# Optimization experiments

Measured on AMD Instinct MI355X. Metric: run time of the kernel, lower is better.

## Reference

```python
import jax, jax.numpy as jnp
import numpy as np

N, E = 50000, 600000
DIN, H, DOUT = 128, 128, 64


def setup_inputs() -> dict:
    key = jax.random.key(0)
    ks = jax.random.split(key, 8)
    x = jax.random.normal(ks[0], (N, DIN), dtype=jnp.float32)
    edge_index = jax.random.randint(ks[1], (2, E), 0, N, dtype=jnp.int64)
    s1 = 1.0 / np.sqrt(DIN)
    s2 = 1.0 / np.sqrt(H)
    # PyG SAGEConv: lin_l (on aggregated neighbors, with bias), lin_r (on root, no bias)
    w1_l = jax.random.uniform(ks[2], (DIN, H), jnp.float32, -s1, s1)
    b1 = jnp.zeros((H,), jnp.float32)
    w1_r = jax.random.uniform(ks[3], (DIN, H), jnp.float32, -s1, s1)
    w2_l = jax.random.uniform(ks[4], (H, DOUT), jnp.float32, -s2, s2)
    b2 = jnp.zeros((DOUT,), jnp.float32)
    w2_r = jax.random.uniform(ks[5], (H, DOUT), jnp.float32, -s2, s2)
    return {"x": x, "edge_index": edge_index, "w1_l": w1_l, "b1": b1,
            "w1_r": w1_r, "w2_l": w2_l, "b2": b2, "w2_r": w2_r}


def _sage_conv(h, src, dst, w_l, b, w_r):
    # mean-aggregate neighbor features: gather by src, scatter-sum to dst
    agg = jax.ops.segment_sum(h[src], dst, num_segments=N)  # [N, d]
    deg = jax.ops.segment_sum(jnp.ones((src.shape[0],), h.dtype), dst,
                              num_segments=N)
    mean = agg / jnp.maximum(deg, 1.0)[:, None]
    return mean @ w_l + b + h @ w_r


def reference(x, edge_index, w1_l, b1, w1_r, w2_l, b2, w2_r):
    src, dst = edge_index[0], edge_index[1]
    h = jax.nn.relu(_sage_conv(x, src, dst, w1_l, b1, w1_r))
    return _sage_conv(h, src, dst, w2_l, b2, w2_r)
```

## Files before the change

kernel.cpp:

```cpp
#include <hip/hip_runtime.h>

#define N_NODES 50000
#define N_EDGES 600000
#define DIN 128
#define HD 128
#define DOUT 64
#define NBINS 196
#define BUFCAP 32
#define MAXBIN 6144

typedef float f32x4 __attribute__((ext_vector_type(4)));
typedef short bf16x8 __attribute__((ext_vector_type(8)));

__device__ __forceinline__ unsigned short f2bf(float f) {
    unsigned u = __float_as_uint(f);
    unsigned r = (u + 0x7FFFu + ((u >> 16) & 1u)) >> 16;
    return (unsigned short)r;
}

__global__ __launch_bounds__(256) void cursorinit_kernel(int* __restrict__ binCursor) {
    if (threadIdx.x < NBINS) binCursor[threadIdx.x] = threadIdx.x * MAXBIN;
}

__global__ __launch_bounds__(256) void mega_kernel(const int* __restrict__ ei,
                                                   int* __restrict__ binCursor,
                                                   unsigned* __restrict__ gbuf,
                                                   const float* __restrict__ x,
                                                   unsigned short* __restrict__ xb,
                                                   const float* __restrict__ w1l,
                                                   const float* __restrict__ w1r,
                                                   const float* __restrict__ w2l,
                                                   const float* __restrict__ w2r,
                                                   unsigned short* __restrict__ bfr) {
    int gid = blockIdx.x;
    if (gid < 256) {
        __shared__ unsigned buf[NBINS][BUFCAP];
        __shared__ int cnt[NBINS];
        for (int i = threadIdx.x; i < NBINS; i += 256) cnt[i] = 0;
        __syncthreads();
        const int per = (N_EDGES + 255) / 256;
        int beg = gid * per;
        int end = min(beg + per, N_EDGES);
        for (int base = beg; base < end; base += 256) {
            int e = base + threadIdx.x;
            if (e < end) {
                int s = ei[e];
                int d = ei[N_EDGES + e];
                int bin = d >> 8;
                unsigned entry = ((unsigned)(d & 255) << 17) | (unsigned)s;
                int pos = atomicAdd(&cnt[bin], 1);
                if (pos < BUFCAP) buf[bin][pos] = entry;
                else { int g = atomicAdd(&binCursor[bin], 1); gbuf[g] = entry; }
            }
            __syncthreads();
            if (threadIdx.x < NBINS) {
                int b = threadIdx.x;
                int n = cnt[b]; if (n > BUFCAP) n = BUFCAP;
                int k = n & ~15;
                if (k > 0) {
                    int g = atomicAdd(&binCursor[b], k);
                    for (int j = 0; j < k; j++) gbuf[g + j] = buf[b][j];
                    for (int j = 0; j < n - k; j++) buf[b][j] = buf[b][k + j];
                    cnt[b] = n - k;
                } else {
                    cnt[b] = n;
                }
            }
            __syncthreads();
        }
        if (threadIdx.x < NBINS) {
            int b = threadIdx.x;
            int n = cnt[b]; if (n > BUFCAP) n = BUFCAP;
            if (n > 0) {
                int g = atomicAdd(&binCursor[b], n);
                for (int j = 0; j < n; j++) gbuf[g + j] = buf[b][j];
            }
        }
    } else if (gid < 6506) {
        int i = (gid - 256) * 256 + threadIdx.x;
        float4 v = ((const float4*)x)[i];
        ushort4 o;
        o.x = f2bf(v.x); o.y = f2bf(v.y); o.z = f2bf(v.z); o.w = f2bf(v.w);
        ((ushort4*)xb)[i] = o;
    } else {
        int tid = (gid - 6506) * 256 + threadIdx.x;
        int a = tid >> 14;
        int r = tid & 16383;
        int j = r & 7, lane = (r >> 3) & 63, kc = (r >> 9) & 3, ct = r >> 11;
        int k = kc * 32 + ((lane >> 4) << 3) + j;
        int c = (ct << 4) + (lane & 15);
        float v;
        if (a == 0) v = w1l[k * HD + c];
        else if (a == 1) v = w1r[k * HD + c];
        else v = (c < 64) ? w2l[k * DOUT + c] : w2r[k * DOUT + (c - 64)];
        bfr[tid] = f2bf(v);
    }
}

__global__ __launch_bounds__(256) void binsort_kernel(unsigned* __restrict__ gbuf,
                                                      const int* __restrict__ binCursor,
                                                      int* __restrict__ row_ptr,
                                                      int* __restrict__ row_end) {
    __shared__ unsigned ebuf[MAXBIN];
    __shared__ int hist[256];
    __shared__ int cur[256];
    __shared__ int ws[4];
    const int bin = blockIdx.x;
    const int base = bin * MAXBIN;
    int n = binCursor[bin] - base;
    if (n > MAXBIN) n = MAXBIN;
    unsigned* src = gbuf + base;
    for (int i = threadIdx.x; i < n; i += 256) ebuf[i] = src[i];
    hist[threadIdx.x] = 0;
    __syncthreads();
    for (int i = threadIdx.x; i < n; i += 256) atomicAdd(&hist[ebuf[i] >> 17], 1);
    __syncthreads();
    const int lane = threadIdx.x & 63, wid = threadIdx.x >> 6;
    int v = hist[threadIdx.x];
    int incl = v;
#pragma unroll
    for (int off = 1; off < 64; off <<= 1) {
        int t = __shfl_up(incl, (unsigned)off, 64);
        if (lane >= off) incl += t;
    }
    if (lane == 63) ws[wid] = incl;
    __syncthreads();
    int woff = 0;
    for (int w = 0; w < wid; w++) woff += ws[w];
    int excl = woff + incl - v;
    cur[threadIdx.x] = excl;
    int node = bin * 256 + threadIdx.x;
    if (node < N_NODES) {
        row_ptr[node] = base + excl;
        row_end[node] = base + excl + v;
    }
    __syncthreads();
    for (int i = threadIdx.x; i < n; i += 256) {
        unsigned e = ebuf[i];
        int pos = atomicAdd(&cur[e >> 17], 1);
        src[pos] = e & 0x1FFFFu;
    }
}

__global__ __launch_bounds__(256) void gather1_kernel(const int* __restrict__ row_ptr,
                                                      const int* __restrict__ row_end,
                                                      const int* __restrict__ csr,
                                                      const unsigned short* __restrict__ xb,
                                                      unsigned short* __restrict__ meanb) {
    int node = blockIdx.x * 4 + (threadIdx.x >> 6);
    if (node >= N_NODES) return;
    const int lane = threadIdx.x & 63;
    const int g = lane >> 4;
    const int sl = lane & 15;
    int beg = row_ptr[node], end = row_end[node];
    float acc[8] = {0.f, 0.f, 0.f, 0.f, 0.f, 0.f, 0.f, 0.f};
    for (int base = beg + g; base < end; base += 12) {
        int i1 = base + 4, i2 = base + 8;
        int s0 = csr[base];
        int s1 = csr[i1 < end ? i1 : base];
        int s2 = csr[i2 < end ? i2 : base];
        uint4 u0 = *(const uint4*)(xb + (size_t)s0 * DIN + sl * 8);
        uint4 u1 = *(const uint4*)(xb + (size_t)s1 * DIN + sl * 8);
        uint4 u2 = *(const uint4*)(xb + (size_t)s2 * DIN + sl * 8);
        if (i1 >= end) u1 = (uint4){0u, 0u, 0u, 0u};
        if (i2 >= end) u2 = (uint4){0u, 0u, 0u, 0u};
        acc[0] += __uint_as_float(u0.x << 16) + __uint_as_float(u1.x << 16) + __uint_as_float(u2.x << 16);
        acc[1] += __uint_as_float(u0.x & 0xffff0000u) + __uint_as_float(u1.x & 0xffff0000u) + __uint_as_float(u2.x & 0xffff0000u);
        acc[2] += __uint_as_float(u0.y << 16) + __uint_as_float(u1.y << 16) + __uint_as_float(u2.y << 16);
        acc[3] += __uint_as_float(u0.y & 0xffff0000u) + __uint_as_float(u1.y & 0xffff0000u) + __uint_as_float(u2.y & 0xffff0000u);
        acc[4] += __uint_as_float(u0.z << 16) + __uint_as_float(u1.z << 16) + __uint_as_float(u2.z << 16);
        acc[5] += __uint_as_float(u0.z & 0xffff0000u) + __uint_as_float(u1.z & 0xffff0000u) + __uint_as_float(u2.z & 0xffff0000u);
        acc[6] += __uint_as_float(u0.w << 16) + __uint_as_float(u1.w << 16) + __uint_as_float(u2.w << 16);
        acc[7] += __uint_as_float(u0.w & 0xffff0000u) + __uint_as_float(u1.w & 0xffff0000u) + __uint_as_float(u2.w & 0xffff0000u);
    }
#pragma unroll
    for (int i = 0; i < 8; i++) {
        acc[i] += __shfl_xor(acc[i], 16, 64);
        acc[i] += __shfl_xor(acc[i], 32, 64);
    }
    float r0, r1;
    if (g == 0)      { r0 = acc[0]; r1 = acc[1]; }
    else if (g == 1) { r0 = acc[2]; r1 = acc[3]; }
    else if (g == 2) { r0 = acc[4]; r1 = acc[5]; }
    else             { r0 = acc[6]; r1 = acc[7]; }
    float invd = 1.0f / fmaxf((float)(end - beg), 1.0f);
    ushort2 r; r.x = f2bf(r0 * invd); r.y = f2bf(r1 * invd);
    *(ushort2*)(meanb + (size_t)node * DIN + sl * 8 + g * 2) = r;
}

__global__ __launch_bounds__(256) void fused_kernel(
    const unsigned short* __restrict__ meanb, const unsigned short* __restrict__ xb,
    const unsigned short* __restrict__ B1a, const unsigned short* __restrict__ B1b,
    const unsigned short* __restrict__ B2,
    const float* __restrict__ b1, const float* __restrict__ b2,
    unsigned short* __restrict__ pb, float* __restrict__ out) {
    __shared__ unsigned short Am[64 * 128];
    __shared__ unsigned short Ax[64 * 128];
    const int block0 = blockIdx.x * 64;
    const int tid = threadIdx.x;
    const int lane = tid & 63;
    const int wtile = tid >> 6;

    uint4 mv[4], xv[4];
#pragma unroll
    for (int i = 0; i < 4; i++) {
        int f = tid + i * 256;
        int row = f >> 4;
        int c8 = f & 15;
        int rg = block0 + row;
        if (rg >= N_NODES) rg = N_NODES - 1;
        mv[i] = *(const uint4*)(meanb + (size_t)rg * DIN + c8 * 8);
        xv[i] = *(const uint4*)(xb + (size_t)rg * DIN + c8 * 8);
    }

    f32x4 acc[8];
#pragma unroll
    for (int t = 0; t < 8; t++) acc[t] = (f32x4){0.f, 0.f, 0.f, 0.f};

#pragma unroll
    for (int i = 0; i < 4; i++) {
        int f = tid + i * 256;
        int row = f >> 4;
        int c8 = f & 15;
        int byte = row * 256 + ((c8 * 16) ^ ((row & 7) << 4));
        *(uint4*)((char*)Am + byte) = mv[i];
        *(uint4*)((char*)Ax + byte) = xv[i];
    }

    auto compute = [&](const unsigned short* __restrict__ As,
                       const unsigned short* __restrict__ Bf) {
        const int arow = wtile * 16 + (lane & 15);
        const int swz = (arow & 7) << 4;
#pragma unroll
        for (int kc = 0; kc < 4; kc++) {
            int byte = arow * 256 + ((kc * 64 + ((lane >> 4) << 4)) ^ swz);
            bf16x8 a = *(const bf16x8*)((const char*)As + byte);
#pragma unroll
            for (int ct = 0; ct < 8; ct++) {
                bf16x8 b = *(const bf16x8*)(Bf + ((((ct << 2) + kc) << 6) + lane) * 8);
                acc[ct] = __builtin_amdgcn_mfma_f32_16x16x32_bf16(a, b, acc[ct], 0, 0, 0);
            }
        }
    };

    __syncthreads();
    compute(Am, B1a);
    compute(Ax, B1b);

    {
        const int r0 = wtile * 16 + ((lane >> 4) << 2);
#pragma unroll
        for (int ct = 0; ct < 8; ct++) {
            int col = (ct << 4) + (lane & 15);
            float bv = b1[col];
#pragma unroll
            for (int r = 0; r < 4; r++) {
                float v = fmaxf(acc[ct][r] + bv, 0.f);
                int row = r0 + r;
                int byte = row * 256 + ((col * 2) ^ ((row & 7) << 4));
                *(unsigned short*)((char*)Am + byte) = f2bf(v);
            }
            acc[ct] = (f32x4){0.f, 0.f, 0.f, 0.f};
        }
    }
    compute(Am, B2);

    {
        const int r0 = wtile * 16 + ((lane >> 4) << 2);
#pragma unroll
        for (int ct = 0; ct < 8; ct++) {
            int col = (ct << 4) + (lane & 15);
#pragma unroll
            for (int r = 0; r < 4; r++) {
                int node = block0 + r0 + r;
                if (node < N_NODES) {
                    if (ct < 4) pb[(size_t)node * DOUT + col] = f2bf(acc[ct][r]);
                    else out[(size_t)node * DOUT + (col - 64)] = acc[ct][r] + b2[col - 64];
                }
            }
        }
    }
}

__global__ __launch_bounds__(256) void gather2_kernel(const int* __restrict__ row_ptr,
                                                      const int* __restrict__ row_end,
                                                      const int* __restrict__ csr,
                                                      const unsigned short* __restrict__ pb,
                                                      float* __restrict__ out) {
    int node = blockIdx.x * 4 + (threadIdx.x >> 6);
    if (node >= N_NODES) return;
    const int lane = threadIdx.x & 63;
    const int g = lane >> 3;
    const int sl = lane & 7;
    int beg = row_ptr[node], end = row_end[node];
    float acc[8] = {0.f, 0.f, 0.f, 0.f, 0.f, 0.f, 0.f, 0.f};
    for (int base = beg + g; base < end; base += 16) {
        int i1 = base + 8;
        int s0 = csr[base];
        int s1 = csr[i1 < end ? i1 : base];
        uint4 u0 = *(const uint4*)(pb + (size_t)s0 * DOUT + sl * 8);
        uint4 u1 = *(const uint4*)(pb + (size_t)s1 * DOUT + sl * 8);
        if (i1 >= end) u1 = (uint4){0u, 0u, 0u, 0u};
        acc[0] += __uint_as_float(u0.x << 16) + __uint_as_float(u1.x << 16);
        acc[1] += __uint_as_float(u0.x & 0xffff0000u) + __uint_as_float(u1.x & 0xffff0000u);
        acc[2] += __uint_as_float(u0.y << 16) + __uint_as_float(u1.y << 16);
        acc[3] += __uint_as_float(u0.y & 0xffff0000u) + __uint_as_float(u1.y & 0xffff0000u);
        acc[4] += __uint_as_float(u0.z << 16) + __uint_as_float(u1.z << 16);
        acc[5] += __uint_as_float(u0.z & 0xffff0000u) + __uint_as_float(u1.z & 0xffff0000u);
        acc[6] += __uint_as_float(u0.w << 16) + __uint_as_float(u1.w << 16);
        acc[7] += __uint_as_float(u0.w & 0xffff0000u) + __uint_as_float(u1.w & 0xffff0000u);
    }
#pragma unroll
    for (int i = 0; i < 8; i++) {
        acc[i] += __shfl_xor(acc[i], 8, 64);
        acc[i] += __shfl_xor(acc[i], 16, 64);
        acc[i] += __shfl_xor(acc[i], 32, 64);
    }
    float r;
    if (g == 0)      r = acc[0];
    else if (g == 1) r = acc[1];
    else if (g == 2) r = acc[2];
    else if (g == 3) r = acc[3];
    else if (g == 4) r = acc[4];
    else if (g == 5) r = acc[5];
    else if (g == 6) r = acc[6];
    else             r = acc[7];
    float invd = 1.0f / fmaxf((float)(end - beg), 1.0f);
    int d = sl * 8 + g;
    out[(size_t)node * DOUT + d] += r * invd;
}

extern "C" void kernel_launch(void* const* d_in, const int* in_sizes, int n_in,
                              void* d_out, int out_size, void* d_ws, size_t ws_size,
                              hipStream_t stream) {
    const float* x   = (const float*)d_in[0];
    const int*   ei  = (const int*)d_in[1];
    const float* w1l = (const float*)d_in[2];
    const float* b1  = (const float*)d_in[3];
    const float* w1r = (const float*)d_in[4];
    const float* w2l = (const float*)d_in[5];
    const float* b2  = (const float*)d_in[6];
    const float* w2r = (const float*)d_in[7];
    float* out = (float*)d_out;

    int* iw = (int*)d_ws;
    int* binCursor = iw;
    int* row_ptr   = iw + 256;
    int* row_end   = iw + 50256;
    unsigned* gbuf = (unsigned*)(iw + 100352);
    unsigned short* meanb = (unsigned short*)(iw + 1304576);
    unsigned short* xb  = meanb + (size_t)N_NODES * DIN;
    unsigned short* pbb = xb + (size_t)N_NODES * DIN;
    unsigned short* bfr = pbb + (size_t)N_NODES * DOUT;
    const unsigned short* B1a = bfr;
    const unsigned short* B1b = bfr + 16384;
    const unsigned short* B2  = bfr + 32768;

    cursorinit_kernel<<<1, 256, 0, stream>>>(binCursor);
    mega_kernel<<<6698, 256, 0, stream>>>(ei, binCursor, gbuf, x, xb,
                                          w1l, w1r, w2l, w2r, bfr);
    binsort_kernel<<<NBINS, 256, 0, stream>>>(gbuf, binCursor, row_ptr, row_end);

    gather1_kernel<<<(N_NODES + 3) / 4, 256, 0, stream>>>(row_ptr, row_end,
                                                          (const int*)gbuf, xb, meanb);
    fused_kernel<<<(N_NODES + 63) / 64, 256, 0, stream>>>(meanb, xb, B1a, B1b, B2,
                                                          b1, b2, pbb, out);
    gather2_kernel<<<(N_NODES + 3) / 4, 256, 0, stream>>>(row_ptr, row_end,
                                                          (const int*)gbuf, pbb, out);
}
```

Baseline: 115.4 us.

## Fuse layer-1 neighbor mean gather into the fused GEMM kernel

Removes the separate gather1 kernel and has each block of the fused GEMM kernel compute the neighbor means for its 64 nodes, writing bf16 results directly into shared memory. Each wave processes its 16 nodes two at a time to keep more loads in flight. This avoids writing and rereading the intermediate mean buffer and saves a launch. In exchange, gather work runs with far fewer blocks in flight, which may expose gather latency.

```diff
diff --git a/kernel.cpp b/kernel.cpp
--- a/kernel.cpp
+++ b/kernel.cpp
@@ -142,54 +142,9 @@
     }
 }
 
-__global__ __launch_bounds__(256) void gather1_kernel(const int* __restrict__ row_ptr,
-                                                      const int* __restrict__ row_end,
-                                                      const int* __restrict__ csr,
-                                                      const unsigned short* __restrict__ xb,
-                                                      unsigned short* __restrict__ meanb) {
-    int node = blockIdx.x * 4 + (threadIdx.x >> 6);
-    if (node >= N_NODES) return;
-    const int lane = threadIdx.x & 63;
-    const int g = lane >> 4;
-    const int sl = lane & 15;
-    int beg = row_ptr[node], end = row_end[node];
-    float acc[8] = {0.f, 0.f, 0.f, 0.f, 0.f, 0.f, 0.f, 0.f};
-    for (int base = beg + g; base < end; base += 12) {
-        int i1 = base + 4, i2 = base + 8;
-        int s0 = csr[base];
-        int s1 = csr[i1 < end ? i1 : base];
-        int s2 = csr[i2 < end ? i2 : base];
-        uint4 u0 = *(const uint4*)(xb + (size_t)s0 * DIN + sl * 8);
-        uint4 u1 = *(const uint4*)(xb + (size_t)s1 * DIN + sl * 8);
-        uint4 u2 = *(const uint4*)(xb + (size_t)s2 * DIN + sl * 8);
-        if (i1 >= end) u1 = (uint4){0u, 0u, 0u, 0u};
-        if (i2 >= end) u2 = (uint4){0u, 0u, 0u, 0u};
-        acc[0] += __uint_as_float(u0.x << 16) + __uint_as_float(u1.x << 16) + __uint_as_float(u2.x << 16);
-        acc[1] += __uint_as_float(u0.x & 0xffff0000u) + __uint_as_float(u1.x & 0xffff0000u) + __uint_as_float(u2.x & 0xffff0000u);
-        acc[2] += __uint_as_float(u0.y << 16) + __uint_as_float(u1.y << 16) + __uint_as_float(u2.y << 16);
-        acc[3] += __uint_as_float(u0.y & 0xffff0000u) + __uint_as_float(u1.y & 0xffff0000u) + __uint_as_float(u2.y & 0xffff0000u);
-        acc[4] += __uint_as_float(u0.z << 16) + __uint_as_float(u1.z << 16) + __uint_as_float(u2.z << 16);
-        acc[5] += __uint_as_float(u0.z & 0xffff0000u) + __uint_as_float(u1.z & 0xffff0000u) + __uint_as_float(u2.z & 0xffff0000u);
-        acc[6] += __uint_as_float(u0.w << 16) + __uint_as_float(u1.w << 16) + __uint_as_float(u2.w << 16);
-        acc[7] += __uint_as_float(u0.w & 0xffff0000u) + __uint_as_float(u1.w & 0xffff0000u) + __uint_as_float(u2.w & 0xffff0000u);
-    }
-#pragma unroll
-    for (int i = 0; i < 8; i++) {
-        acc[i] += __shfl_xor(acc[i], 16, 64);
-        acc[i] += __shfl_xor(acc[i], 32, 64);
-    }
-    float r0, r1;
-    if (g == 0)      { r0 = acc[0]; r1 = acc[1]; }
-    else if (g == 1) { r0 = acc[2]; r1 = acc[3]; }
-    else if (g == 2) { r0 = acc[4]; r1 = acc[5]; }
-    else             { r0 = acc[6]; r1 = acc[7]; }
-    float invd = 1.0f / fmaxf((float)(end - beg), 1.0f);
-    ushort2 r; r.x = f2bf(r0 * invd); r.y = f2bf(r1 * invd);
-    *(ushort2*)(meanb + (size_t)node * DIN + sl * 8 + g * 2) = r;
-}
-
-__global__ __launch_bounds__(256) void fused_kernel(
-    const unsigned short* __restrict__ meanb, const unsigned short* __restrict__ xb,
+__global__ __launch_bounds__(256) void fusedG_kernel(
+    const int* __restrict__ row_ptr, const int* __restrict__ row_end,
+    const int* __restrict__ csr, const unsigned short* __restrict__ xb,
     const unsigned short* __restrict__ B1a, const unsigned short* __restrict__ B1b,
     const unsigned short* __restrict__ B2,
     const float* __restrict__ b1, const float* __restrict__ b2,
@@ -201,7 +156,7 @@
     const int lane = tid & 63;
     const int wtile = tid >> 6;
 
-    uint4 mv[4], xv[4];
+    uint4 xv[4];
 #pragma unroll
     for (int i = 0; i < 4; i++) {
         int f = tid + i * 256;
@@ -209,8 +164,80 @@
         int c8 = f & 15;
         int rg = block0 + row;
         if (rg >= N_NODES) rg = N_NODES - 1;
-        mv[i] = *(const uint4*)(meanb + (size_t)rg * DIN + c8 * 8);
         xv[i] = *(const uint4*)(xb + (size_t)rg * DIN + c8 * 8);
+    }
+
+    {
+        const int g = lane >> 4;
+        const int sl = lane & 15;
+        const int nodeBase = block0 + wtile * 16;
+        int rp = 0, re = 0;
+        {
+            int idx = nodeBase + (lane & 15);
+            if (idx < N_NODES) { rp = row_ptr[idx]; re = row_end[idx]; }
+        }
+        const int swzbase = lane * 2;
+
+#define G1STEP(bb, ee, A)                                                     \
+        {                                                                     \
+            int i1 = (bb) + 4, i2 = (bb) + 8;                                 \
+            int s0 = csr[(bb)];                                               \
+            int s1 = csr[i1 < (ee) ? i1 : (bb)];                              \
+            int s2 = csr[i2 < (ee) ? i2 : (bb)];                              \
+            uint4 u0 = *(const uint4*)(xb + (size_t)s0 * DIN + sl * 8);       \
+            uint4 u1 = *(const uint4*)(xb + (size_t)s1 * DIN + sl * 8);       \
+            uint4 u2 = *(const uint4*)(xb + (size_t)s2 * DIN + sl * 8);       \
+            if (i1 >= (ee)) u1 = (uint4){0u, 0u, 0u, 0u};                     \
+            if (i2 >= (ee)) u2 = (uint4){0u, 0u, 0u, 0u};                     \
+            A[0] += __uint_as_float(u0.x << 16) + __uint_as_float(u1.x << 16) + __uint_as_float(u2.x << 16); \
+            A[1] += __uint_as_float(u0.x & 0xffff0000u) + __uint_as_float(u1.x & 0xffff0000u) + __uint_as_float(u2.x & 0xffff0000u); \
+            A[2] += __uint_as_float(u0.y << 16) + __uint_as_float(u1.y << 16) + __uint_as_float(u2.y << 16); \
+            A[3] += __uint_as_float(u0.y & 0xffff0000u) + __uint_as_float(u1.y & 0xffff0000u) + __uint_as_float(u2.y & 0xffff0000u); \
+            A[4] += __uint_as_float(u0.z << 16) + __uint_as_float(u1.z << 16) + __uint_as_float(u2.z << 16); \
+            A[5] += __uint_as_float(u0.z & 0xffff0000u) + __uint_as_float(u1.z & 0xffff0000u) + __uint_as_float(u2.z & 0xffff0000u); \
+            A[6] += __uint_as_float(u0.w << 16) + __uint_as_float(u1.w << 16) + __uint_as_float(u2.w << 16); \
+            A[7] += __uint_as_float(u0.w & 0xffff0000u) + __uint_as_float(u1.w & 0xffff0000u) + __uint_as_float(u2.w & 0xffff0000u); \
+        }
+
+        for (int i = 0; i < 16; i += 2) {
+            int begA = __shfl(rp, i, 64), endA = __shfl(re, i, 64);
+            int begB = __shfl(rp, i + 1, 64), endB = __shfl(re, i + 1, 64);
+            float accA[8] = {0.f, 0.f, 0.f, 0.f, 0.f, 0.f, 0.f, 0.f};
+            float accB[8] = {0.f, 0.f, 0.f, 0.f, 0.f, 0.f, 0.f, 0.f};
+            int baseA = begA + g, baseB = begB + g;
+            while (baseA < endA && baseB < endB) {
+                G1STEP(baseA, endA, accA);
+                G1STEP(baseB, endB, accB);
+                baseA += 12; baseB += 12;
+            }
+            while (baseA < endA) { G1STEP(baseA, endA, accA); baseA += 12; }
+            while (baseB < endB) { G1STEP(baseB, endB, accB); baseB += 12; }
+#pragma unroll
+            for (int k = 0; k < 8; k++) {
+                accA[k] += __shfl_xor(accA[k], 16, 64);
+                accA[k] += __shfl_xor(accA[k], 32, 64);
+                accB[k] += __shfl_xor(accB[k], 16, 64);
+                accB[k] += __shfl_xor(accB[k], 32, 64);
+            }
+            float rA0, rA1, rB0, rB1;
+            if (g == 0)      { rA0 = accA[0]; rA1 = accA[1]; rB0 = accB[0]; rB1 = accB[1]; }
+            else if (g == 1) { rA0 = accA[2]; rA1 = accA[3]; rB0 = accB[2]; rB1 = accB[3]; }
+            else if (g == 2) { rA0 = accA[4]; rA1 = accA[5]; rB0 = accB[4]; rB1 = accB[5]; }
+            else             { rA0 = accA[6]; rA1 = accA[7]; rB0 = accB[6]; rB1 = accB[7]; }
+            float invdA = 1.0f / fmaxf((float)(endA - begA), 1.0f);
+            float invdB = 1.0f / fmaxf((float)(endB - begB), 1.0f);
+            int rowA = wtile * 16 + i;
+            int rowB = rowA + 1;
+            int colb = sl * 16 + g * 4;
+            int byteA = rowA * 256 + (((sl * 16) ^ ((rowA & 7) << 4)) + g * 4);
+            int byteB = rowB * 256 + (((sl * 16) ^ ((rowB & 7) << 4)) + g * 4);
+            ushort2 oA; oA.x = f2bf(rA0 * invdA); oA.y = f2bf(rA1 * invdA);
+            ushort2 oB; oB.x = f2bf(rB0 * invdB); oB.y = f2bf(rB1 * invdB);
+            *(ushort2*)((char*)Am + byteA) = oA;
+            *(ushort2*)((char*)Am + byteB) = oB;
+            (void)colb;
+        }
+#undef G1STEP
     }
 
     f32x4 acc[8];
@@ -223,7 +250,6 @@
         int row = f >> 4;
         int c8 = f & 15;
         int byte = row * 256 + ((c8 * 16) ^ ((row & 7) << 4));
-        *(uint4*)((char*)Am + byte) = mv[i];
         *(uint4*)((char*)Ax + byte) = xv[i];
     }
 
@@ -348,8 +374,7 @@
     int* row_ptr   = iw + 256;
     int* row_end   = iw + 50256;
     unsigned* gbuf = (unsigned*)(iw + 100352);
-    unsigned short* meanb = (unsigned short*)(iw + 1304576);
-    unsigned short* xb  = meanb + (size_t)N_NODES * DIN;
+    unsigned short* xb  = (unsigned short*)(iw + 1304576);
     unsigned short* pbb = xb + (size_t)N_NODES * DIN;
     unsigned short* bfr = pbb + (size_t)N_NODES * DOUT;
     const unsigned short* B1a = bfr;
@@ -361,10 +386,10 @@
                                           w1l, w1r, w2l, w2r, bfr);
     binsort_kernel<<<NBINS, 256, 0, stream>>>(gbuf, binCursor, row_ptr, row_end);
 
-    gather1_kernel<<<(N_NODES + 3) / 4, 256, 0, stream>>>(row_ptr, row_end,
-                                                          (const int*)gbuf, xb, meanb);
-    fused_kernel<<<(N_NODES + 63) / 64, 256, 0, stream>>>(meanb, xb, B1a, B1b, B2,
-                                                          b1, b2, pbb, out);
+    fusedG_kernel<<<(N_NODES + 63) / 64, 256, 0, stream>>>(row_ptr, row_end,
+                                                           (const int*)gbuf, xb,
+                                                           B1a, B1b, B2, b1, b2,
+                                                           pbb, out);
     gather2_kernel<<<(N_NODES + 3) / 4, 256, 0, stream>>>(row_ptr, row_end,
                                                           (const int*)gbuf, pbb, out);
 }
```

Result: slower. 137.0 us (+18.6%).
